# Optimization experiments

Hardware: AMD Instinct MI355X
Metric: run time of the kernel (lower is better)

Reference implementation:

```python
import jax, jax.numpy as jnp
import numpy as np

B, NQ, NK = 4, 2048, 2048
DQ = DK = DV = 512
H = 8
DS = DV // H  # 64


def _layernorm(x, g, b, eps=1e-5):
    m = jnp.mean(x, axis=-1, keepdims=True)
    v = jnp.var(x, axis=-1, keepdims=True)
    return (x - m) * jax.lax.rsqrt(v + eps) * g + b


def setup_inputs() -> dict:
    key = jax.random.key(0)
    ks = jax.random.split(key, 16)
    def lin(k, fan_in, fan_out):
        # torch nn.Linear default init: U(-1/sqrt(fan_in), 1/sqrt(fan_in))
        bound = 1.0 / np.sqrt(fan_in)
        k1, k2 = jax.random.split(k)
        W = jax.random.uniform(k1, (fan_in, fan_out), jnp.float32, -bound, bound)
        b = jax.random.uniform(k2, (fan_out,), jnp.float32, -bound, bound)
        return W, b
    Wq, bq = lin(ks[0], DQ, DV)
    Wk, bk = lin(ks[1], DK, DV)
    Wv, bv = lin(ks[2], DK, DV)
    W0, b0 = lin(ks[3], DV, DV)
    W1, b1 = lin(ks[4], DV, DV)
    # xavier_uniform for kp/vp of shape (1, DS): bound = sqrt(6/(1+DS))
    xb = np.sqrt(6.0 / (1 + DS))
    kp = jax.random.uniform(ks[5], (DS,), jnp.float32, -xb, xb)
    vp = jax.random.uniform(ks[6], (DS,), jnp.float32, -xb, xb)
    return {
        "Q": jax.random.normal(ks[7], (B, NQ, DQ), jnp.float32),
        "K": jax.random.normal(ks[8], (B, NK, DK), jnp.float32),
        "Kpos": jax.random.uniform(ks[9], (B, NQ, NK), jnp.float32),
        "Wq": Wq, "bq": bq, "Wk": Wk, "bk": bk, "Wv": Wv, "bv": bv,
        "kp": kp, "vp": vp,
        "W0": W0, "b0": b0, "W1": W1, "b1": b1,
        "g0": jnp.ones((DV,), jnp.float32), "be0": jnp.zeros((DV,), jnp.float32),
        "g1": jnp.ones((DV,), jnp.float32), "be1": jnp.zeros((DV,), jnp.float32),
    }


def reference(Q, K, Kpos, Wq, bq, Wk, bk, Wv, bv, kp, vp, W0, b0, W1, b1, g0, be0, g1, be1):
    Qp = Q @ Wq + bq                       # [B,NQ,DV]
    Kp = K @ Wk + bk                       # [B,NK,DV]
    Vp = K @ Wv + bv                       # [B,NK,DV]
    # head split (torch split/cat along batch == reshape to [B,N,H,DS])
    Qh = Qp.reshape(B, NQ, H, DS)
    Kh = Kp.reshape(B, NK, H, DS)
    Vh = Vp.reshape(B, NK, H, DS)
    scale = 1.0 / np.sqrt(DV)              # NOTE: original scales by sqrt(dim_V), not per-head dim
    scores = jnp.einsum('bqhd,bkhd->bhqk', Qh, Kh) * scale
    # ShawRE key bias: KE[b,h,q,k] = Kpos[b,q,k] * <Qh[b,q,h,:], kp>
    qkp = jnp.einsum('bqhd,d->bhq', Qh, kp)          # [B,H,NQ]
    scores = scores + Kpos[:, None, :, :] * qkp[:, :, :, None]
    A = jax.nn.softmax(scores, axis=-1)              # [B,H,NQ,NK]
    out = jnp.einsum('bhqk,bkhd->bqhd', A, Vh)       # [B,NQ,H,DS]
    # ShawRE value bias: VE[b,q,h,:] = (sum_k A*Kpos) * vp
    akp = jnp.einsum('bhqk,bqk->bhq', A, Kpos)       # [B,H,NQ]
    out = out + akp.transpose(0, 2, 1)[..., None] * vp
    O = (Qh + out).reshape(B, NQ, DV)
    O = _layernorm(O, g0, be0)
    resO = O
    O = jax.nn.relu(O @ W0 + b0)           # fc_o[0] with relu (numlayers=2)
    O = resO + jax.nn.relu(O @ W1 + b1)    # fc_o[-1] + residual
    O = _layernorm(O, g1, be1)
    return O
```

## Files before the change

kernel.cpp:

```cpp
#include <hip/hip_runtime.h>
#include <math.h>

#define Bx  4
#define NQx 2048
#define NKx 2048
#define Dx  512
#define Hx  8

typedef __attribute__((ext_vector_type(8))) __bf16 bf16x8;
typedef __attribute__((ext_vector_type(4))) float f32x4;
typedef __attribute__((ext_vector_type(16))) float f32x16;

typedef const __attribute__((address_space(1))) unsigned int* gas_ptr;
typedef __attribute__((address_space(3))) unsigned int* lds_ptr;

__device__ __forceinline__ void gload16(const void* g, void* l){
  __builtin_amdgcn_global_load_lds((gas_ptr)g, (lds_ptr)l, 16, 0, 0);
}

__device__ __forceinline__ unsigned short f2bf(float f){
  union { float f; unsigned int u; } v; v.f = f;
  unsigned int r = (v.u + 0x7FFFu + ((v.u >> 16) & 1u)) >> 16;
  return (unsigned short)r;
}
__device__ __forceinline__ float bf2f(unsigned short u){
  union { unsigned int u; float f; } v; v.u = ((unsigned int)u) << 16; return v.f;
}
__device__ __forceinline__ unsigned int cvtpk_bf16(float a, float b){
  unsigned int d;
  asm("v_cvt_pk_bf16_f32 %0, %1, %2" : "=v"(d) : "v"(a), "v"(b));
  return d;
}
__device__ __forceinline__ void plane32_swap(unsigned int& a, unsigned int& b){
  asm("v_permlane32_swap_b32 %0, %1" : "+v"(a), "+v"(b));
}
__device__ __forceinline__ float fexp2(float x){
  float d; asm("v_exp_f32 %0, %1" : "=v"(d) : "v"(x)); return d;
}
__device__ __forceinline__ float fmax3(float a, float b, float c){
  float d; asm("v_max3_f32 %0, %1, %2, %3" : "=v"(d) : "v"(a), "v"(b), "v"(c)); return d;
}

__global__ __launch_bounds__(256) void mab_wt(
    const float* __restrict__ Wq, const float* __restrict__ Wk, const float* __restrict__ Wv,
    const float* __restrict__ W0, const float* __restrict__ W1,
    unsigned short* __restrict__ Wt)
{
  __shared__ unsigned short T[64][72];
  const int z = blockIdx.z;
  const float* W = (z==0)?Wq:(z==1)?Wk:(z==2)?Wv:(z==3)?W0:W1;
  unsigned short* O = Wt + (size_t)z*512*512;
  const int k0 = blockIdx.x*64, n0 = blockIdx.y*64;
  const int tid = threadIdx.x;
  #pragma unroll
  for (int i=0;i<4;++i){
    int id = tid + i*256;
    int r = id>>4, c4 = id&15;
    float4 v = *(const float4*)(W + (size_t)(k0+r)*512 + n0 + c4*4);
    ushort4 o; o.x=f2bf(v.x); o.y=f2bf(v.y); o.z=f2bf(v.z); o.w=f2bf(v.w);
    *(ushort4*)&T[r][c4*4] = o;
  }
  __syncthreads();
  #pragma unroll
  for (int i=0;i<2;++i){
    int id = tid + i*256;
    int c = id>>3, r8 = id&7;
    union { unsigned short u[8]; uint4 v; } o;
    #pragma unroll
    for (int j=0;j<8;++j) o.u[j] = T[r8*8+j][c];
    *(uint4*)(O + (size_t)(n0+c)*512 + k0 + r8*8) = o.v;
  }
}

__global__ __launch_bounds__(256) void mab_vt(
    const unsigned short* __restrict__ Vp, unsigned short* __restrict__ Vpt)
{
  __shared__ unsigned short T[64][72];
  const int r0 = blockIdx.x*64;
  const int c0 = blockIdx.y*64;
  const int b  = blockIdx.z;
  const int tid = threadIdx.x;
  #pragma unroll
  for (int i=0;i<2;++i){
    int id = tid + i*256;
    int r = id>>3, c8 = id&7;
    *(uint4*)&T[r][c8*8] = *(const uint4*)(Vp + (size_t)(b*NKx + r0+r)*512 + c0 + c8*8);
  }
  __syncthreads();
  #pragma unroll
  for (int i=0;i<2;++i){
    int id = tid + i*256;
    int c = id>>3, r8 = id&7;
    union { unsigned short u[8]; uint4 v; } o;
    #pragma unroll
    for (int j=0;j<8;++j) o.u[j] = T[r8*8+j][c];
    *(uint4*)(Vpt + ((size_t)(b*512) + c0 + c)*NKx + r0 + r8*8) = o.v;
  }
}

__global__ __launch_bounds__(256) void mab_gemm_proj(
    const float* __restrict__ Qf, const float* __restrict__ Kf,
    const unsigned short* __restrict__ Wt,
    const float* __restrict__ bq, const float* __restrict__ bk, const float* __restrict__ bv,
    unsigned short* __restrict__ Cb, float kscale)
{
  __shared__ unsigned short As[128][64];
  __shared__ unsigned short Bs[128][64];
  const int z = blockIdx.z;
  const float* A = (z==0) ? Qf : Kf;
  const unsigned short* W = Wt + (size_t)z*512*512;
  const float* bias = (z==0)?bq:((z==1)?bk:bv);
  const float sc = (z==1) ? kscale : 1.0f;
  const int m0 = blockIdx.y*128, n0 = blockIdx.x*128;
  const int tid = threadIdx.x, w = tid>>6, lane = tid&63, g = lane>>4, q16 = lane&15;
  const int wr = w>>1, wc = w&1;

  f32x4 acc[4][4];
  #pragma unroll
  for (int m=0;m<4;++m)
    #pragma unroll
    for (int n=0;n<4;++n) acc[m][n] = (f32x4){0.f,0.f,0.f,0.f};

  float4 areg[8];
  #pragma unroll
  for (int i=0;i<8;++i){
    int id = i*256 + tid, row = id>>4, qc = id&15;
    areg[i] = *(const float4*)(A + (size_t)(m0+row)*512 + qc*4);
  }

  for (int k0 = 0; k0 < 512; k0 += 64){
    __syncthreads();
    #pragma unroll
    for (int i=0;i<8;++i){
      int id = i*256 + tid, row = id>>4, qc = id&15;
      unsigned int lo = cvtpk_bf16(areg[i].x, areg[i].y);
      unsigned int hi = cvtpk_bf16(areg[i].z, areg[i].w);
      unsigned int* dst = (unsigned int*)((char*)&As[0][0] + row*128
                          + ((qc>>1) ^ (row&7))*16 + (qc&1)*8);
      dst[0] = lo; dst[1] = hi;
    }
    #pragma unroll
    for (int i=0;i<4;++i){
      int o   = (w*4 + i)*1024 + lane*16;
      int row = o >> 7;
      int c   = (o >> 4) & 7;
      int cs  = c ^ (row & 7);
      gload16(W + (size_t)(n0+row)*512 + k0 + cs*8, (char*)&Bs[0][0] + (w*4+i)*1024);
    }
    __syncthreads();
    if (k0 + 64 < 512){
      #pragma unroll
      for (int i=0;i<8;++i){
        int id = i*256 + tid, row = id>>4, qc = id&15;
        areg[i] = *(const float4*)(A + (size_t)(m0+row)*512 + (k0+64) + qc*4);
      }
    }
    #pragma unroll
    for (int ks=0;ks<2;++ks){
      bf16x8 af[4], bfr[4];
      #pragma unroll
      for (int m=0;m<4;++m){
        int row = wr*64 + m*16 + q16;
        int c   = (ks*4 + g) ^ (row & 7);
        af[m] = *(const bf16x8*)((const char*)&As[0][0] + row*128 + c*16);
      }
      #pragma unroll
      for (int n=0;n<4;++n){
        int row = wc*64 + n*16 + q16;
        int c   = (ks*4 + g) ^ (row & 7);
        bfr[n] = *(const bf16x8*)((const char*)&Bs[0][0] + row*128 + c*16);
      }
      #pragma unroll
      for (int m=0;m<4;++m)
        #pragma unroll
        for (int n=0;n<4;++n)
          acc[m][n] = __builtin_amdgcn_mfma_f32_16x16x32_bf16(af[m], bfr[n], acc[m][n], 0,0,0);
    }
  }

  const size_t ZS = (size_t)8192*512;
  #pragma unroll
  for (int m=0;m<4;++m){
    const int rowl = wr*64 + m*16 + g*4;
    #pragma unroll
    for (int n=0;n<4;++n){
      const int col = n0 + wc*64 + n*16 + q16;
      const float bv2 = bias[col];
      #pragma unroll
      for (int r=0;r<4;++r){
        float v = (acc[m][n][r] + bv2) * sc;
        Cb[(size_t)z*ZS + (size_t)(m0 + rowl + r)*512 + col] = f2bf(v);
      }
    }
  }
}

__global__ __launch_bounds__(256) void mab_gemm_mfma(
    const unsigned short* __restrict__ A, const unsigned short* __restrict__ W,
    const float* __restrict__ bias, const float* __restrict__ res,
    unsigned short* __restrict__ Cb, float* __restrict__ Cf, int relu)
{
  __shared__ unsigned short As[128][64];
  __shared__ unsigned short Bs[128][64];
  const int m0 = blockIdx.y*128, n0 = blockIdx.x*128;
  const int tid = threadIdx.x, w = tid>>6, lane = tid&63, g = lane>>4, q16 = lane&15;
  const int wr = w>>1, wc = w&1;

  f32x4 acc[4][4];
  #pragma unroll
  for (int m=0;m<4;++m)
    #pragma unroll
    for (int n=0;n<4;++n) acc[m][n] = (f32x4){0.f,0.f,0.f,0.f};

  for (int k0 = 0; k0 < 512; k0 += 64){
    __syncthreads();
    #pragma unroll
    for (int i=0;i<4;++i){
      int o   = (w*4 + i)*1024 + lane*16;
      int row = o >> 7;
      int c   = (o >> 4) & 7;
      int cs  = c ^ (row & 7);
      gload16(A + (size_t)(m0+row)*512 + k0 + cs*8, (char*)&As[0][0] + (w*4+i)*1024);
      gload16(W + (size_t)(n0+row)*512 + k0 + cs*8, (char*)&Bs[0][0] + (w*4+i)*1024);
    }
    __syncthreads();
    #pragma unroll
    for (int ks=0;ks<2;++ks){
      bf16x8 af[4], bfr[4];
      #pragma unroll
      for (int m=0;m<4;++m){
        int row = wr*64 + m*16 + q16;
        int c   = (ks*4 + g) ^ (row & 7);
        af[m] = *(const bf16x8*)((const char*)&As[0][0] + row*128 + c*16);
      }
      #pragma unroll
      for (int n=0;n<4;++n){
        int row = wc*64 + n*16 + q16;
        int c   = (ks*4 + g) ^ (row & 7);
        bfr[n] = *(const bf16x8*)((const char*)&Bs[0][0] + row*128 + c*16);
      }
      #pragma unroll
      for (int m=0;m<4;++m)
        #pragma unroll
        for (int n=0;n<4;++n)
          acc[m][n] = __builtin_amdgcn_mfma_f32_16x16x32_bf16(af[m], bfr[n], acc[m][n], 0,0,0);
    }
  }

  #pragma unroll
  for (int m=0;m<4;++m){
    const int rowl = wr*64 + m*16 + g*4;
    #pragma unroll
    for (int n=0;n<4;++n){
      const int col = n0 + wc*64 + n*16 + q16;
      const float bv = bias[col];
      #pragma unroll
      for (int r=0;r<4;++r){
        float v = acc[m][n][r] + bv;
        if (relu) v = fmaxf(v, 0.f);
        size_t off = (size_t)(m0 + rowl + r)*512 + col;
        if (res) v += res[off];
        if (Cb) Cb[off] = f2bf(v);
        if (Cf) Cf[off] = v;
      }
    }
  }
}

__global__ __launch_bounds__(256) void mab_attn2(
    const unsigned short* __restrict__ Qp, const unsigned short* __restrict__ Kp,
    const unsigned short* __restrict__ Vpt,
    const float* __restrict__ Kpos, const float* __restrict__ kp, const float* __restrict__ vp,
    float* __restrict__ X)
{
  __shared__ unsigned short Kb[2][64][64];
  __shared__ unsigned short Vb[2][64][64];
  __shared__ unsigned short Qs[128][72];

  const int q0 = blockIdx.x*128;
  const int h  = blockIdx.y;
  const int b  = blockIdx.z;
  const int tid = threadIdx.x, w = tid>>6, lane = tid&63;
  const int q32 = lane & 31, hi = lane >> 5;

  const unsigned short* Qg = Qp + ((size_t)(b*NQx + q0))*Dx + h*64;
  const unsigned short* Kg = Kp + ((size_t)b*NKx)*Dx + h*64;
  const unsigned short* Vg = Vpt + ((size_t)(b*512) + h*64)*NKx;
  const float* KProw = Kpos + (size_t)b*NQx*NKx + (size_t)(q0 + w*32 + q32)*NKx;

  const int sr = lane>>3;
  const int sc = lane&7;

  #pragma unroll
  for (int i=0;i<2;++i){
    int r  = i*8 + sr;
    int cs = sc ^ (r & 7);
    gload16(Kg + (size_t)(w*16 + r)*Dx + cs*8, (char*)&Kb[0][0][0] + w*2048 + i*1024);
    gload16(Vg + (size_t)(w*16 + r)*NKx + cs*8, (char*)&Vb[0][0][0] + w*2048 + i*1024);
  }
  f32x4 kq[2][4];
  #pragma unroll
  for (int n=0;n<2;++n)
    #pragma unroll
    for (int a=0;a<4;++a)
      kq[n][a] = *(const f32x4*)(KProw + n*32 + a*8 + hi*4);
  #pragma unroll
  for (int i=0;i<4;++i){
    int id = tid + i*256;
    int r = id>>3, c8 = id&7;
    *(uint4*)&Qs[r][c8*8] = *(const uint4*)(Qg + (size_t)r*Dx + c8*8);
  }
  __syncthreads();

  bf16x8 qf[4];
  #pragma unroll
  for (int ds=0; ds<4; ++ds)
    qf[ds] = *(const bf16x8*)&Qs[w*32 + q32][ds*16 + hi*8];

  float qkp = 0.f;
  #pragma unroll
  for (int ds=0; ds<4; ++ds){
    union { bf16x8 v; unsigned short u[8]; } qa; qa.v = qf[ds];
    #pragma unroll
    for (int j=0;j<8;++j)
      qkp = fmaf(bf2f(qa.u[j]), kp[ds*16 + hi*8 + j], qkp);
  }
  qkp += __shfl_xor(qkp, 32);
  qkp *= 1.4426950408889634f;

  float m_i = -1e30f, l_i = 0.f, a_i = 0.f;
  f32x16 accT[2];
  #pragma unroll
  for (int db=0; db<2; ++db)
    #pragma unroll
    for (int r=0;r<16;++r) accT[db][r] = 0.f;

  const int NT = NKx/64;

  for (int kt = 0; kt < NT; ++kt){
    const int cur = kt & 1;
    const int k0 = kt*64;

    if (kt+1 < NT){
      const int k1 = k0 + 64;
      #pragma unroll
      for (int i=0;i<2;++i){
        int r  = i*8 + sr;
        int cs = sc ^ (r & 7);
        gload16(Kg + (size_t)(k1 + w*16 + r)*Dx + cs*8,
                (char*)&Kb[cur^1][0][0] + w*2048 + i*1024);
        gload16(Vg + (size_t)(w*16 + r)*NKx + k1 + cs*8,
                (char*)&Vb[cur^1][0][0] + w*2048 + i*1024);
      }
    }
    __builtin_amdgcn_sched_barrier(0);

    f32x16 sT[2];
    __builtin_amdgcn_s_setprio(1);
    #pragma unroll
    for (int n=0;n<2;++n){
      f32x16 c;
      #pragma unroll
      for (int r=0;r<16;++r) c[r] = 0.f;
      #pragma unroll
      for (int ds=0; ds<4; ++ds){
        int row = n*32 + q32;
        int cc  = (ds*2 + hi) ^ (q32 & 7);
        bf16x8 kf = *(const bf16x8*)((const char*)&Kb[cur][0][0] + row*128 + cc*16);
        c = __builtin_amdgcn_mfma_f32_32x32x16_bf16(kf, qf[ds], c, 0,0,0);
      }
      sT[n] = c;
    }
    __builtin_amdgcn_s_setprio(0);

    #pragma unroll
    for (int n=0;n<2;++n)
      #pragma unroll
      for (int r=0;r<16;++r)
        sT[n][r] = fmaf(kq[n][r>>2][r&3], qkp, sT[n][r]);

    float m0a = fmax3(sT[0][0], sT[0][1], sT[0][2]);
    float m0b = fmax3(sT[0][3], sT[0][4], sT[0][5]);
    float m0c = fmax3(sT[0][6], sT[0][7], sT[0][8]);
    float m0d = fmax3(sT[0][9], sT[0][10], sT[0][11]);
    float m0e = fmax3(sT[0][12], sT[0][13], sT[0][14]);
    float m1a = fmax3(sT[1][0], sT[1][1], sT[1][2]);
    float m1b = fmax3(sT[1][3], sT[1][4], sT[1][5]);
    float m1c = fmax3(sT[1][6], sT[1][7], sT[1][8]);
    float m1d = fmax3(sT[1][9], sT[1][10], sT[1][11]);
    float m1e = fmax3(sT[1][12], sT[1][13], sT[1][14]);
    float rm = fmax3(fmax3(m0a, m0b, m0c), fmax3(m0d, m0e, sT[0][15]),
                     fmax3(fmax3(m1a, m1b, m1c), fmax3(m1d, m1e, sT[1][15]), m_i));
    rm = fmaxf(rm, __shfl_xor(rm, 32));

    if (!__all(rm <= m_i + 11.544f)){
      float al = fexp2(m_i - rm);
      m_i = rm;
      l_i *= al; a_i *= al;
      #pragma unroll
      for (int db=0; db<2; ++db)
        #pragma unroll
        for (int r=0;r<16;++r) accT[db][r] *= al;
    }

    float ps = 0.f, pk = 0.f;
    #pragma unroll
    for (int n=0;n<2;++n)
      #pragma unroll
      for (int r=0;r<16;++r){
        float p = fexp2(sT[n][r] - m_i);
        sT[n][r] = p;
        ps += p;
        pk = fmaf(p, kq[n][r>>2][r&3], pk);
      }

    {
      const int kn = (kt+1 < NT) ? (k0 + 64) : k0;
      #pragma unroll
      for (int n=0;n<2;++n)
        #pragma unroll
        for (int a=0;a<4;++a)
          kq[n][a] = *(const f32x4*)(KProw + kn + n*32 + a*8 + hi*4);
    }

    ps += __shfl_xor(ps, 32);
    pk += __shfl_xor(pk, 32);
    l_i += ps; a_i += pk;

    union PW { unsigned int u[4]; bf16x8 v; } pa[4];
    #pragma unroll
    for (int n=0;n<2;++n){
      unsigned int w0 = cvtpk_bf16(sT[n][0],  sT[n][1]);
      unsigned int w1 = cvtpk_bf16(sT[n][2],  sT[n][3]);
      unsigned int w2 = cvtpk_bf16(sT[n][4],  sT[n][5]);
      unsigned int w3 = cvtpk_bf16(sT[n][6],  sT[n][7]);
      unsigned int w4 = cvtpk_bf16(sT[n][8],  sT[n][9]);
      unsigned int w5 = cvtpk_bf16(sT[n][10], sT[n][11]);
      unsigned int w6 = cvtpk_bf16(sT[n][12], sT[n][13]);
      unsigned int w7 = cvtpk_bf16(sT[n][14], sT[n][15]);
      plane32_swap(w0, w2);
      plane32_swap(w1, w3);
      plane32_swap(w4, w6);
      plane32_swap(w5, w7);
      pa[n*2+0].u[0]=w0; pa[n*2+0].u[1]=w1; pa[n*2+0].u[2]=w2; pa[n*2+0].u[3]=w3;
      pa[n*2+1].u[0]=w4; pa[n*2+1].u[1]=w5; pa[n*2+1].u[2]=w6; pa[n*2+1].u[3]=w7;
    }

    __builtin_amdgcn_s_setprio(1);
    #pragma unroll
    for (int st=0; st<4; ++st){
      #pragma unroll
      for (int db=0; db<2; ++db){
        int row = db*32 + q32;
        int cc  = (st*2 + hi) ^ (q32 & 7);
        bf16x8 vf = *(const bf16x8*)((const char*)&Vb[cur][0][0] + row*128 + cc*16);
        accT[db] = __builtin_amdgcn_mfma_f32_32x32x16_bf16(vf, pa[st].v, accT[db], 0,0,0);
      }
    }
    __builtin_amdgcn_s_setprio(0);

    asm volatile("s_waitcnt vmcnt(8)" ::: "memory");
    __builtin_amdgcn_s_barrier();
  }

  float inv = 1.0f / l_i;
  float aw  = a_i * inv;
  float* Xrow = X + ((size_t)(b*NQx + q0 + w*32 + q32))*Dx + h*64;
  #pragma unroll
  for (int db=0; db<2; ++db){
    #pragma unroll
    for (int a=0; a<4; ++a){
      int d0 = db*32 + a*8 + hi*4;
      f32x4 vpv = *(const f32x4*)(vp + d0);
      float4 o;
      o.x = fmaf(accT[db][a*4+0], inv, bf2f(Qs[w*32+q32][d0+0]) + aw*vpv[0]);
      o.y = fmaf(accT[db][a*4+1], inv, bf2f(Qs[w*32+q32][d0+1]) + aw*vpv[1]);
      o.z = fmaf(accT[db][a*4+2], inv, bf2f(Qs[w*32+q32][d0+2]) + aw*vpv[2]);
      o.w = fmaf(accT[db][a*4+3], inv, bf2f(Qs[w*32+q32][d0+3]) + aw*vpv[3]);
      *(float4*)(Xrow + d0) = o;
    }
  }
}

__global__ __launch_bounds__(256) void mab_ln2(
    const float* __restrict__ Xin, const float* __restrict__ g,
    const float* __restrict__ be, float* __restrict__ Yf, unsigned short* __restrict__ Yb)
{
  const int row = blockIdx.x;
  const int tid = threadIdx.x;
  const float* x = Xin + (size_t)row*Dx;
  float2 v = *(const float2*)(x + tid*2);
  float s  = v.x + v.y;
  float sq = fmaf(v.x,v.x, v.y*v.y);
  #pragma unroll
  for (int m=1; m<64; m<<=1){ s += __shfl_xor(s,m); sq += __shfl_xor(sq,m); }
  __shared__ float red[2][4];
  const int wid = tid>>6, lane = tid&63;
  if (lane==0){ red[0][wid]=s; red[1][wid]=sq; }
  __syncthreads();
  s  = red[0][0]+red[0][1]+red[0][2]+red[0][3];
  sq = red[1][0]+red[1][1]+red[1][2]+red[1][3];
  float mean = s*(1.0f/Dx);
  float var  = sq*(1.0f/Dx) - mean*mean;
  float rstd = rsqrtf(var + 1e-5f);
  float2 gg = *(const float2*)(g  + tid*2);
  float2 bb = *(const float2*)(be + tid*2);
  float2 o;
  o.x = (v.x-mean)*rstd*gg.x + bb.x;
  o.y = (v.y-mean)*rstd*gg.y + bb.y;
  if (Yf) *(float2*)(Yf + (size_t)row*Dx + tid*2) = o;
  if (Yb){
    ushort2 ob; ob.x = f2bf(o.x); ob.y = f2bf(o.y);
    *(ushort2*)(Yb + (size_t)row*Dx + tid*2) = ob;
  }
}

extern "C" void kernel_launch(void* const* d_in, const int* in_sizes, int n_in,
                              void* d_out, int out_size, void* d_ws, size_t ws_size,
                              hipStream_t stream)
{
  const float* Q    = (const float*)d_in[0];
  const float* K    = (const float*)d_in[1];
  const float* Kpos = (const float*)d_in[2];
  const float* Wq   = (const float*)d_in[3];
  const float* bq   = (const float*)d_in[4];
  const float* Wk   = (const float*)d_in[5];
  const float* bk   = (const float*)d_in[6];
  const float* Wv   = (const float*)d_in[7];
  const float* bv   = (const float*)d_in[8];
  const float* kp   = (const float*)d_in[9];
  const float* vp   = (const float*)d_in[10];
  const float* W0   = (const float*)d_in[11];
  const float* b0   = (const float*)d_in[12];
  const float* W1   = (const float*)d_in[13];
  const float* b1   = (const float*)d_in[14];
  const float* g0   = (const float*)d_in[15];
  const float* be0  = (const float*)d_in[16];
  const float* g1   = (const float*)d_in[17];
  const float* be1  = (const float*)d_in[18];
  float* out = (float*)d_out;
  char* wsb  = (char*)d_ws;

  const size_t MB = 1024*1024;
  unsigned short* Qp  = (unsigned short*)(wsb);
  unsigned short* Kp  = (unsigned short*)(wsb + 8*MB);
  unsigned short* Vp  = (unsigned short*)(wsb + 16*MB);
  float*          O0  = (float*)         (wsb + 24*MB);
  unsigned short* Vpt = (unsigned short*)(wsb + 40*MB);
  unsigned short* O0b = (unsigned short*)(wsb + 48*MB);
  unsigned short* Wt  = (unsigned short*)(wsb + 56*MB);
  unsigned short* T1  = Vp;

  const float kscale = 0.044194173824159216f * 1.4426950408889634f;

  mab_wt<<<dim3(8,8,5), 256, 0, stream>>>(Wq, Wk, Wv, W0, W1, Wt);
  mab_gemm_proj<<<dim3(4,64,3), 256, 0, stream>>>(Q, K, Wt, bq, bk, bv, Qp, kscale);
  mab_vt<<<dim3(32,8,4), 256, 0, stream>>>(Vp, Vpt);
  mab_attn2<<<dim3(16,8,4), 256, 0, stream>>>(Qp, Kp, Vpt, Kpos, kp, vp, out);
  mab_ln2<<<8192, 256, 0, stream>>>(out, g0, be0, O0, O0b);
  mab_gemm_mfma<<<dim3(4,64,1), 256, 0, stream>>>(
      O0b, Wt + (size_t)3*512*512, b0, nullptr, T1, nullptr, 1);
  mab_gemm_mfma<<<dim3(4,64,1), 256, 0, stream>>>(
      T1, Wt + (size_t)4*512*512, b1, O0, nullptr, out, 1);
  mab_ln2<<<8192, 256, 0, stream>>>(out, g1, be1, out, nullptr);
}
```

Measured before the change: 210.0 us.

## Split attention key range across wave pairs and merge partial softmax states

```diff
diff --git a/kernel.cpp b/kernel.cpp
--- a/kernel.cpp
+++ b/kernel.cpp
@@ -267,55 +267,50 @@
   }
 }
 
-__global__ __launch_bounds__(256) void mab_attn2(
+__global__ __launch_bounds__(256, 4) void mab_attn3(
     const unsigned short* __restrict__ Qp, const unsigned short* __restrict__ Kp,
     const unsigned short* __restrict__ Vpt,
     const float* __restrict__ Kpos, const float* __restrict__ kp, const float* __restrict__ vp,
     float* __restrict__ X)
 {
-  __shared__ unsigned short Kb[2][64][64];
-  __shared__ unsigned short Vb[2][64][64];
-  __shared__ unsigned short Qs[128][72];
-
-  const int q0 = blockIdx.x*128;
+  __shared__ __align__(16) char pool[32768];
+
+  const int q0 = blockIdx.x*64;
   const int h  = blockIdx.y;
   const int b  = blockIdx.z;
   const int tid = threadIdx.x, w = tid>>6, lane = tid&63;
   const int q32 = lane & 31, hi = lane >> 5;
+  const int g = w>>1;
+  const int qrow = (w&1)*32 + q32;
+
+  char* Kbase = pool + g*16384;
+  char* Vbase = pool + g*16384 + 8192;
 
   const unsigned short* Qg = Qp + ((size_t)(b*NQx + q0))*Dx + h*64;
   const unsigned short* Kg = Kp + ((size_t)b*NKx)*Dx + h*64;
   const unsigned short* Vg = Vpt + ((size_t)(b*512) + h*64)*NKx;
-  const float* KProw = Kpos + (size_t)b*NQx*NKx + (size_t)(q0 + w*32 + q32)*NKx;
-
-  const int sr = lane>>3;
-  const int sc = lane&7;
+  const float* KProw = Kpos + (size_t)b*NQx*NKx + (size_t)(q0 + qrow)*NKx;
+
+  const int krow0 = lane>>3, kch = lane&7;
+  const int vrow0 = lane>>2, vch = lane&3;
+  const int shalf = (w&1)*2;
 
   #pragma unroll
   for (int i=0;i<2;++i){
-    int r  = i*8 + sr;
-    int cs = sc ^ (r & 7);
-    gload16(Kg + (size_t)(w*16 + r)*Dx + cs*8, (char*)&Kb[0][0][0] + w*2048 + i*1024);
-    gload16(Vg + (size_t)(w*16 + r)*NKx + cs*8, (char*)&Vb[0][0][0] + w*2048 + i*1024);
-  }
-  f32x4 kq[2][4];
-  #pragma unroll
-  for (int n=0;n<2;++n)
-    #pragma unroll
-    for (int a=0;a<4;++a)
-      kq[n][a] = *(const f32x4*)(KProw + n*32 + a*8 + hi*4);
-  #pragma unroll
-  for (int i=0;i<4;++i){
-    int id = tid + i*256;
-    int r = id>>3, c8 = id&7;
-    *(uint4*)&Qs[r][c8*8] = *(const uint4*)(Qg + (size_t)r*Dx + c8*8);
-  }
-  __syncthreads();
-
+    int s = shalf + i;
+    int kr = s*8 + krow0;
+    int kcs = kch ^ (kr & 7);
+    gload16(Kg + (size_t)(g*32 + kr)*Dx + kcs*8, Kbase + s*1024);
+    int vr = s*16 + vrow0;
+    int vcs = vch ^ ((vr>>1) & 3);
+    gload16(Vg + (size_t)vr*NKx + g*32 + vcs*8, Vbase + s*1024);
+  }
+
+  const unsigned short* Qrowp = Qg + (size_t)qrow*Dx;
   bf16x8 qf[4];
   #pragma unroll
   for (int ds=0; ds<4; ++ds)
-    qf[ds] = *(const bf16x8*)&Qs[w*32 + q32][ds*16 + hi*8];
+    qf[ds] = *(const bf16x8*)(Qrowp + ds*16 + hi*8);
 
   float qkp = 0.f;
   #pragma unroll
@@ -335,62 +330,54 @@
     #pragma unroll
     for (int r=0;r<16;++r) accT[db][r] = 0.f;
 
-  const int NT = NKx/64;
-
-  for (int kt = 0; kt < NT; ++kt){
-    const int cur = kt & 1;
-    const int k0 = kt*64;
-
-    if (kt+1 < NT){
-      const int k1 = k0 + 64;
+  __syncthreads();
+
+  for (int t = 0; t < 32; ++t){
+    const int cur = t & 1;
+    const int k0g = t*64 + g*32;
+
+    f32x4 kq[4];
+    #pragma unroll
+    for (int a=0;a<4;++a)
+      kq[a] = *(const f32x4*)(KProw + k0g + a*8 + hi*4);
+
+    if (t < 31){
+      const int k1 = k0g + 64;
       #pragma unroll
       for (int i=0;i<2;++i){
-        int r  = i*8 + sr;
-        int cs = sc ^ (r & 7);
-        gload16(Kg + (size_t)(k1 + w*16 + r)*Dx + cs*8,
-                (char*)&Kb[cur^1][0][0] + w*2048 + i*1024);
-        gload16(Vg + (size_t)(w*16 + r)*NKx + k1 + cs*8,
-                (char*)&Vb[cur^1][0][0] + w*2048 + i*1024);
+        int s = shalf + i;
+        int kr = s*8 + krow0;
+        int kcs = kch ^ (kr & 7);
+        gload16(Kg + (size_t)(k1 + kr)*Dx + kcs*8, Kbase + (cur^1)*4096 + s*1024);
+        int vr = s*16 + vrow0;
+        int vcs = vch ^ ((vr>>1) & 3);
+        gload16(Vg + (size_t)vr*NKx + k1 + vcs*8, Vbase + (cur^1)*4096 + s*1024);
       }
     }
     __builtin_amdgcn_sched_barrier(0);
 
-    f32x16 sT[2];
+    f32x16 sT;
+    #pragma unroll
+    for (int r=0;r<16;++r) sT[r] = 0.f;
     __builtin_amdgcn_s_setprio(1);
     #pragma unroll
-    for (int n=0;n<2;++n){
-      f32x16 c;
-      #pragma unroll
-      for (int r=0;r<16;++r) c[r] = 0.f;
-      #pragma unroll
-      for (int ds=0; ds<4; ++ds){
-        int row = n*32 + q32;
-        int cc  = (ds*2 + hi) ^ (q32 & 7);
-        bf16x8 kf = *(const bf16x8*)((const char*)&Kb[cur][0][0] + row*128 + cc*16);
-        c = __builtin_amdgcn_mfma_f32_32x32x16_bf16(kf, qf[ds], c, 0,0,0);
-      }
-      sT[n] = c;
+    for (int ds=0; ds<4; ++ds){
+      int cc = (ds*2 + hi) ^ (q32 & 7);
+      bf16x8 kf = *(const bf16x8*)(Kbase + cur*4096 + q32*128 + cc*16);
+      sT = __builtin_amdgcn_mfma_f32_32x32x16_bf16(kf, qf[ds], sT, 0,0,0);
     }
     __builtin_amdgcn_s_setprio(0);
 
     #pragma unroll
-    for (int n=0;n<2;++n)
-      #pragma unroll
-      for (int r=0;r<16;++r)
-        sT[n][r] = fmaf(kq[n][r>>2][r&3], qkp, sT[n][r]);
-
-    float m0a = fmax3(sT[0][0], sT[0][1], sT[0][2]);
-    float m0b = fmax3(sT[0][3], sT[0][4], sT[0][5]);
-    float m0c = fmax3(sT[0][6], sT[0][7], sT[0][8]);
-    float m0d = fmax3(sT[0][9], sT[0][10], sT[0][11]);
-    float m0e = fmax3(sT[0][12], sT[0][13], sT[0][14]);
-    float m1a = fmax3(sT[1][0], sT[1][1], sT[1][2]);
-    float m1b = fmax3(sT[1][3], sT[1][4], sT[1][5]);
-    float m1c = fmax3(sT[1][6], sT[1][7], sT[1][8]);
-    float m1d = fmax3(sT[1][9], sT[1][10], sT[1][11]);
-    float m1e = fmax3(sT[1][12], sT[1][13], sT[1][14]);
-    float rm = fmax3(fmax3(m0a, m0b, m0c), fmax3(m0d, m0e, sT[0][15]),
-                     fmax3(fmax3(m1a, m1b, m1c), fmax3(m1d, m1e, sT[1][15]), m_i));
+    for (int r=0;r<16;++r)
+      sT[r] = fmaf(kq[r>>2][r&3], qkp, sT[r]);
+
+    float p0 = fmax3(sT[0],  sT[1],  sT[2]);
+    float p1 = fmax3(sT[3],  sT[4],  sT[5]);
+    float p2 = fmax3(sT[6],  sT[7],  sT[8]);
+    float p3 = fmax3(sT[9],  sT[10], sT[11]);
+    float p4 = fmax3(sT[12], sT[13], sT[14]);
+    float rm = fmax3(fmax3(p0, p1, p2), fmax3(p3, p4, sT[15]), m_i);
     rm = fmaxf(rm, __shfl_xor(rm, 32));
 
     if (!__all(rm <= m_i + 11.544f)){
@@ -405,78 +392,82 @@
 
     float ps = 0.f, pk = 0.f;
     #pragma unroll
-    for (int n=0;n<2;++n)
-      #pragma unroll
-      for (int r=0;r<16;++r){
-        float p = fexp2(sT[n][r] - m_i);
-        sT[n][r] = p;
-        ps += p;
-        pk = fmaf(p, kq[n][r>>2][r&3], pk);
-      }
-
-    {
-      const int kn = (kt+1 < NT) ? (k0 + 64) : k0;
-      #pragma unroll
-      for (int n=0;n<2;++n)
-        #pragma unroll
-        for (int a=0;a<4;++a)
-          kq[n][a] = *(const f32x4*)(KProw + kn + n*32 + a*8 + hi*4);
-    }
-
+    for (int r=0;r<16;++r){
+      float p = fexp2(sT[r] - m_i);
+      sT[r] = p;
+      ps += p;
+      pk = fmaf(p, kq[r>>2][r&3], pk);
+    }
     ps += __shfl_xor(ps, 32);
     pk += __shfl_xor(pk, 32);
     l_i += ps; a_i += pk;
 
-    union PW { unsigned int u[4]; bf16x8 v; } pa[4];
-    #pragma unroll
-    for (int n=0;n<2;++n){
-      unsigned int w0 = cvtpk_bf16(sT[n][0],  sT[n][1]);
-      unsigned int w1 = cvtpk_bf16(sT[n][2],  sT[n][3]);
-      unsigned int w2 = cvtpk_bf16(sT[n][4],  sT[n][5]);
-      unsigned int w3 = cvtpk_bf16(sT[n][6],  sT[n][7]);
-      unsigned int w4 = cvtpk_bf16(sT[n][8],  sT[n][9]);
-      unsigned int w5 = cvtpk_bf16(sT[n][10], sT[n][11]);
-      unsigned int w6 = cvtpk_bf16(sT[n][12], sT[n][13]);
-      unsigned int w7 = cvtpk_bf16(sT[n][14], sT[n][15]);
+    union PW { unsigned int u[4]; bf16x8 v; } pa[2];
+    {
+      unsigned int w0 = cvtpk_bf16(sT[0],  sT[1]);
+      unsigned int w1 = cvtpk_bf16(sT[2],  sT[3]);
+      unsigned int w2 = cvtpk_bf16(sT[4],  sT[5]);
+      unsigned int w3 = cvtpk_bf16(sT[6],  sT[7]);
+      unsigned int w4 = cvtpk_bf16(sT[8],  sT[9]);
+      unsigned int w5 = cvtpk_bf16(sT[10], sT[11]);
+      unsigned int w6 = cvtpk_bf16(sT[12], sT[13]);
+      unsigned int w7 = cvtpk_bf16(sT[14], sT[15]);
       plane32_swap(w0, w2);
       plane32_swap(w1, w3);
       plane32_swap(w4, w6);
       plane32_swap(w5, w7);
-      pa[n*2+0].u[0]=w0; pa[n*2+0].u[1]=w1; pa[n*2+0].u[2]=w2; pa[n*2+0].u[3]=w3;
-      pa[n*2+1].u[0]=w4; pa[n*2+1].u[1]=w5; pa[n*2+1].u[2]=w6; pa[n*2+1].u[3]=w7;
+      pa[0].u[0]=w0; pa[0].u[1]=w1; pa[0].u[2]=w2; pa[0].u[3]=w3;
+      pa[1].u[0]=w4; pa[1].u[1]=w5; pa[1].u[2]=w6; pa[1].u[3]=w7;
     }
 
     __builtin_amdgcn_s_setprio(1);
     #pragma unroll
-    for (int st=0; st<4; ++st){
+    for (int c2=0; c2<2; ++c2){
       #pragma unroll
       for (int db=0; db<2; ++db){
         int row = db*32 + q32;
-        int cc  = (st*2 + hi) ^ (q32 & 7);
-        bf16x8 vf = *(const bf16x8*)((const char*)&Vb[cur][0][0] + row*128 + cc*16);
-        accT[db] = __builtin_amdgcn_mfma_f32_32x32x16_bf16(vf, pa[st].v, accT[db], 0,0,0);
+        int cc  = (c2*2 + hi) ^ ((row>>1) & 3);
+        bf16x8 vf = *(const bf16x8*)(Vbase + cur*4096 + row*64 + cc*16);
+        accT[db] = __builtin_amdgcn_mfma_f32_32x32x16_bf16(vf, pa[c2].v, accT[db], 0,0,0);
       }
     }
     __builtin_amdgcn_s_setprio(0);
 
-    asm volatile("s_waitcnt vmcnt(8)" ::: "memory");
-    __builtin_amdgcn_s_barrier();
-  }
-
-  float inv = 1.0f / l_i;
-  float aw  = a_i * inv;
-  float* Xrow = X + ((size_t)(b*NQx + q0 + w*32 + q32))*Dx + h*64;
-  #pragma unroll
-  for (int db=0; db<2; ++db){
-    #pragma unroll
-    for (int a=0; a<4; ++a){
-      int d0 = db*32 + a*8 + hi*4;
+    __syncthreads();
+  }
+
+  __syncthreads();
+  float* mp = (float*)pool;
+  {
+    int slot = w*64 + lane;
+    float* ms = mp + slot*20;
+    int send = 1 - g;
+    #pragma unroll
+    for (int r=0;r<16;++r) ms[r] = accT[send][r];
+    ms[16] = m_i; ms[17] = l_i; ms[18] = a_i;
+  }
+  __syncthreads();
+  {
+    int pslot = (w^2)*64 + lane;
+    const float* pp = mp + pslot*20;
+    float pm = pp[16], pl = pp[17], pav = pp[18];
+    float mM = fmaxf(m_i, pm);
+    float alS = fexp2(m_i - mM), alP = fexp2(pm - mM);
+    float lM = fmaf(l_i, alS, pl*alP);
+    float aM = fmaf(a_i, alS, pav*alP);
+    float inv = 1.0f / lM;
+    float aw  = aM * inv;
+    float* Xrow = X + ((size_t)(b*NQx + q0 + qrow))*Dx + h*64;
+    #pragma unroll
+    for (int a2=0; a2<4; ++a2){
+      int d0 = g*32 + a2*8 + hi*4;
       f32x4 vpv = *(const f32x4*)(vp + d0);
+      ushort4 qh = *(const ushort4*)(Qrowp + d0);
       float4 o;
-      o.x = fmaf(accT[db][a*4+0], inv, bf2f(Qs[w*32+q32][d0+0]) + aw*vpv[0]);
-      o.y = fmaf(accT[db][a*4+1], inv, bf2f(Qs[w*32+q32][d0+1]) + aw*vpv[1]);
-      o.z = fmaf(accT[db][a*4+2], inv, bf2f(Qs[w*32+q32][d0+2]) + aw*vpv[2]);
-      o.w = fmaf(accT[db][a*4+3], inv, bf2f(Qs[w*32+q32][d0+3]) + aw*vpv[3]);
+      o.x = fmaf(fmaf(accT[g][a2*4+0], alS, pp[a2*4+0]*alP), inv, bf2f(qh.x) + aw*vpv[0]);
+      o.y = fmaf(fmaf(accT[g][a2*4+1], alS, pp[a2*4+1]*alP), inv, bf2f(qh.y) + aw*vpv[1]);
+      o.z = fmaf(fmaf(accT[g][a2*4+2], alS, pp[a2*4+2]*alP), inv, bf2f(qh.z) + aw*vpv[2]);
+      o.w = fmaf(fmaf(accT[g][a2*4+3], alS, pp[a2*4+3]*alP), inv, bf2f(qh.w) + aw*vpv[3]);
       *(float4*)(Xrow + d0) = o;
     }
   }
@@ -556,7 +547,7 @@
   mab_wt<<<dim3(8,8,5), 256, 0, stream>>>(Wq, Wk, Wv, W0, W1, Wt);
   mab_gemm_proj<<<dim3(4,64,3), 256, 0, stream>>>(Q, K, Wt, bq, bk, bv, Qp, kscale);
   mab_vt<<<dim3(32,8,4), 256, 0, stream>>>(Vp, Vpt);
-  mab_attn2<<<dim3(16,8,4), 256, 0, stream>>>(Qp, Kp, Vpt, Kpos, kp, vp, out);
+  mab_attn3<<<dim3(32,8,4), 256, 0, stream>>>(Qp, Kp, Vpt, Kpos, kp, vp, out);
   mab_ln2<<<8192, 256, 0, stream>>>(out, g0, be0, O0, O0b);
   mab_gemm_mfma<<<dim3(4,64,1), 256, 0, stream>>>(
       O0b, Wt + (size_t)3*512*512, b0, nullptr, T1, nullptr, 1);
```

Measured after the change: 217.8 us, median of 4. +3.7%, slower.

## Split attention KV loop across two wave groups and merge softmax partials

Applied to the files above, without the earlier changes.

```diff
diff --git a/kernel.cpp b/kernel.cpp
--- a/kernel.cpp
+++ b/kernel.cpp
@@ -267,55 +267,50 @@
   }
 }
 
-__global__ __launch_bounds__(256) void mab_attn2(
+__global__ __launch_bounds__(512, 4) void mab_attn4(
     const unsigned short* __restrict__ Qp, const unsigned short* __restrict__ Kp,
     const unsigned short* __restrict__ Vpt,
     const float* __restrict__ Kpos, const float* __restrict__ kp, const float* __restrict__ vp,
     float* __restrict__ X)
 {
-  __shared__ unsigned short Kb[2][64][64];
-  __shared__ unsigned short Vb[2][64][64];
-  __shared__ unsigned short Qs[128][72];
+  __shared__ __align__(16) char pool[65536];
 
   const int q0 = blockIdx.x*128;
   const int h  = blockIdx.y;
   const int b  = blockIdx.z;
   const int tid = threadIdx.x, w = tid>>6, lane = tid&63;
   const int q32 = lane & 31, hi = lane >> 5;
+  const int qg = w & 3;
+  const int kg = w >> 2;
+  const int qrow = qg*32 + q32;
+
+  char* Kbase = pool + kg*32768;
+  char* Vbase = pool + kg*32768 + 16384;
 
   const unsigned short* Qg = Qp + ((size_t)(b*NQx + q0))*Dx + h*64;
   const unsigned short* Kg = Kp + ((size_t)b*NKx)*Dx + h*64;
   const unsigned short* Vg = Vpt + ((size_t)(b*512) + h*64)*NKx;
-  const float* KProw = Kpos + (size_t)b*NQx*NKx + (size_t)(q0 + w*32 + q32)*NKx;
+  const float* KProw = Kpos + (size_t)b*NQx*NKx + (size_t)(q0 + qrow)*NKx;
 
   const int sr = lane>>3;
   const int sc = lane&7;
 
-  #pragma unroll
-  for (int i=0;i<2;++i){
-    int r  = i*8 + sr;
-    int cs = sc ^ (r & 7);
-    gload16(Kg + (size_t)(w*16 + r)*Dx + cs*8, (char*)&Kb[0][0][0] + w*2048 + i*1024);
-    gload16(Vg + (size_t)(w*16 + r)*NKx + cs*8, (char*)&Vb[0][0][0] + w*2048 + i*1024);
-  }
-  f32x4 kq[2][4];
-  #pragma unroll
-  for (int n=0;n<2;++n)
-    #pragma unroll
-    for (int a=0;a<4;++a)
-      kq[n][a] = *(const f32x4*)(KProw + n*32 + a*8 + hi*4);
-  #pragma unroll
-  for (int i=0;i<4;++i){
-    int id = tid + i*256;
-    int r = id>>3, c8 = id&7;
-    *(uint4*)&Qs[r][c8*8] = *(const uint4*)(Qg + (size_t)r*Dx + c8*8);
-  }
-  __syncthreads();
-
+  {
+    const int k0g = kg*64;
+    #pragma unroll
+    for (int i=0;i<2;++i){
+      int r  = qg*16 + i*8 + sr;
+      int cs = sc ^ (r & 7);
+      gload16(Kg + (size_t)(k0g + r)*Dx + cs*8, Kbase + qg*2048 + i*1024);
+      gload16(Vg + (size_t)r*NKx + k0g + cs*8, Vbase + qg*2048 + i*1024);
+    }
+  }
+
+  const unsigned short* Qrowp = Qg + (size_t)qrow*Dx;
   bf16x8 qf[4];
   #pragma unroll
   for (int ds=0; ds<4; ++ds)
-    qf[ds] = *(const bf16x8*)&Qs[w*32 + q32][ds*16 + hi*8];
+    qf[ds] = *(const bf16x8*)(Qrowp + ds*16 + hi*8);
 
   float qkp = 0.f;
   #pragma unroll
@@ -335,22 +330,29 @@
     #pragma unroll
     for (int r=0;r<16;++r) accT[db][r] = 0.f;
 
-  const int NT = NKx/64;
-
-  for (int kt = 0; kt < NT; ++kt){
-    const int cur = kt & 1;
-    const int k0 = kt*64;
-
-    if (kt+1 < NT){
-      const int k1 = k0 + 64;
+  __syncthreads();
+
+  for (int t = 0; t < 16; ++t){
+    const int cur = t & 1;
+    const int k0g = t*128 + kg*64;
+
+    f32x4 kq[2][4];
+    #pragma unroll
+    for (int n=0;n<2;++n)
+      #pragma unroll
+      for (int a=0;a<4;++a)
+        kq[n][a] = *(const f32x4*)(KProw + k0g + n*32 + a*8 + hi*4);
+
+    if (t < 15){
+      const int k1 = k0g + 128;
       #pragma unroll
       for (int i=0;i<2;++i){
-        int r  = i*8 + sr;
+        int r  = qg*16 + i*8 + sr;
         int cs = sc ^ (r & 7);
-        gload16(Kg + (size_t)(k1 + w*16 + r)*Dx + cs*8,
-                (char*)&Kb[cur^1][0][0] + w*2048 + i*1024);
-        gload16(Vg + (size_t)(w*16 + r)*NKx + k1 + cs*8,
-                (char*)&Vb[cur^1][0][0] + w*2048 + i*1024);
+        gload16(Kg + (size_t)(k1 + r)*Dx + cs*8,
+                Kbase + (cur^1)*8192 + qg*2048 + i*1024);
+        gload16(Vg + (size_t)r*NKx + k1 + cs*8,
+                Vbase + (cur^1)*8192 + qg*2048 + i*1024);
       }
     }
     __builtin_amdgcn_sched_barrier(0);
@@ -366,7 +368,7 @@
       for (int ds=0; ds<4; ++ds){
         int row = n*32 + q32;
         int cc  = (ds*2 + hi) ^ (q32 & 7);
-        bf16x8 kf = *(const bf16x8*)((const char*)&Kb[cur][0][0] + row*128 + cc*16);
+        bf16x8 kf = *(const bf16x8*)(Kbase + cur*8192 + row*128 + cc*16);
         c = __builtin_amdgcn_mfma_f32_32x32x16_bf16(kf, qf[ds], c, 0,0,0);
       }
       sT[n] = c;
@@ -413,16 +415,6 @@
         ps += p;
         pk = fmaf(p, kq[n][r>>2][r&3], pk);
       }
-
-    {
-      const int kn = (kt+1 < NT) ? (k0 + 64) : k0;
-      #pragma unroll
-      for (int n=0;n<2;++n)
-        #pragma unroll
-        for (int a=0;a<4;++a)
-          kq[n][a] = *(const f32x4*)(KProw + kn + n*32 + a*8 + hi*4);
-    }
-
     ps += __shfl_xor(ps, 32);
     pk += __shfl_xor(pk, 32);
     l_i += ps; a_i += pk;
@@ -453,30 +445,46 @@
       for (int db=0; db<2; ++db){
         int row = db*32 + q32;
         int cc  = (st*2 + hi) ^ (q32 & 7);
-        bf16x8 vf = *(const bf16x8*)((const char*)&Vb[cur][0][0] + row*128 + cc*16);
+        bf16x8 vf = *(const bf16x8*)(Vbase + cur*8192 + row*128 + cc*16);
         accT[db] = __builtin_amdgcn_mfma_f32_32x32x16_bf16(vf, pa[st].v, accT[db], 0,0,0);
       }
     }
     __builtin_amdgcn_s_setprio(0);
 
-    asm volatile("s_waitcnt vmcnt(8)" ::: "memory");
-    __builtin_amdgcn_s_barrier();
-  }
-
-  float inv = 1.0f / l_i;
-  float aw  = a_i * inv;
-  float* Xrow = X + ((size_t)(b*NQx + q0 + w*32 + q32))*Dx + h*64;
-  #pragma unroll
-  for (int db=0; db<2; ++db){
-    #pragma unroll
-    for (int a=0; a<4; ++a){
-      int d0 = db*32 + a*8 + hi*4;
+    __syncthreads();
+  }
+
+  float* mp = (float*)pool;
+  {
+    int slot = w*64 + lane;
+    float* ms = mp + slot*20;
+    int send = 1 - kg;
+    #pragma unroll
+    for (int r=0;r<16;++r) ms[r] = accT[send][r];
+    ms[16] = m_i; ms[17] = l_i; ms[18] = a_i;
+  }
+  __syncthreads();
+  {
+    int pslot = (w^4)*64 + lane;
+    const float* pp = mp + pslot*20;
+    float pm = pp[16], pl = pp[17], pav = pp[18];
+    float mM = fmaxf(m_i, pm);
+    float alS = fexp2(m_i - mM), alP = fexp2(pm - mM);
+    float lM = fmaf(l_i, alS, pl*alP);
+    float aM = fmaf(a_i, alS, pav*alP);
+    float inv = 1.0f / lM;
+    float aw  = aM * inv;
+    float* Xrow = X + ((size_t)(b*NQx + q0 + qrow))*Dx + h*64;
+    #pragma unroll
+    for (int a2=0; a2<4; ++a2){
+      int d0 = kg*32 + a2*8 + hi*4;
       f32x4 vpv = *(const f32x4*)(vp + d0);
+      ushort4 qh = *(const ushort4*)(Qrowp + d0);
       float4 o;
-      o.x = fmaf(accT[db][a*4+0], inv, bf2f(Qs[w*32+q32][d0+0]) + aw*vpv[0]);
-      o.y = fmaf(accT[db][a*4+1], inv, bf2f(Qs[w*32+q32][d0+1]) + aw*vpv[1]);
-      o.z = fmaf(accT[db][a*4+2], inv, bf2f(Qs[w*32+q32][d0+2]) + aw*vpv[2]);
-      o.w = fmaf(accT[db][a*4+3], inv, bf2f(Qs[w*32+q32][d0+3]) + aw*vpv[3]);
+      o.x = fmaf(fmaf(accT[kg][a2*4+0], alS, pp[a2*4+0]*alP), inv, bf2f(qh.x) + aw*vpv[0]);
+      o.y = fmaf(fmaf(accT[kg][a2*4+1], alS, pp[a2*4+1]*alP), inv, bf2f(qh.y) + aw*vpv[1]);
+      o.z = fmaf(fmaf(accT[kg][a2*4+2], alS, pp[a2*4+2]*alP), inv, bf2f(qh.z) + aw*vpv[2]);
+      o.w = fmaf(fmaf(accT[kg][a2*4+3], alS, pp[a2*4+3]*alP), inv, bf2f(qh.w) + aw*vpv[3]);
       *(float4*)(Xrow + d0) = o;
     }
   }
@@ -556,7 +564,7 @@
   mab_wt<<<dim3(8,8,5), 256, 0, stream>>>(Wq, Wk, Wv, W0, W1, Wt);
   mab_gemm_proj<<<dim3(4,64,3), 256, 0, stream>>>(Q, K, Wt, bq, bk, bv, Qp, kscale);
   mab_vt<<<dim3(32,8,4), 256, 0, stream>>>(Vp, Vpt);
-  mab_attn2<<<dim3(16,8,4), 256, 0, stream>>>(Qp, Kp, Vpt, Kpos, kp, vp, out);
+  mab_attn4<<<dim3(16,8,4), 512, 0, stream>>>(Qp, Kp, Vpt, Kpos, kp, vp, out);
   mab_ln2<<<8192, 256, 0, stream>>>(out, g0, be0, O0, O0b);
   mab_gemm_mfma<<<dim3(4,64,1), 256, 0, stream>>>(
       O0b, Wt + (size_t)3*512*512, b0, nullptr, T1, nullptr, 1);
```

After: 279.9 us. 33.3% more time.

## Restructure attention so one block covers all heads and shares Kpos through LDS

Applied to the files above, without the earlier changes.

```diff
diff --git a/kernel.cpp b/kernel.cpp
--- a/kernel.cpp
+++ b/kernel.cpp
@@ -267,55 +267,34 @@
   }
 }
 
-__global__ __launch_bounds__(256) void mab_attn2(
+__global__ __launch_bounds__(512, 2) void mab_attn5(
     const unsigned short* __restrict__ Qp, const unsigned short* __restrict__ Kp,
     const unsigned short* __restrict__ Vpt,
     const float* __restrict__ Kpos, const float* __restrict__ kp, const float* __restrict__ vp,
     float* __restrict__ X)
 {
-  __shared__ unsigned short Kb[2][64][64];
-  __shared__ unsigned short Vb[2][64][64];
-  __shared__ unsigned short Qs[128][72];
-
-  const int q0 = blockIdx.x*128;
-  const int h  = blockIdx.y;
-  const int b  = blockIdx.z;
+  __shared__ __align__(16) float KQ[2][2048];
+
+  const int b  = blockIdx.x;
+  const int q0 = blockIdx.y*32;
   const int tid = threadIdx.x, w = tid>>6, lane = tid&63;
   const int q32 = lane & 31, hi = lane >> 5;
+  const int h = w;
 
   const unsigned short* Qg = Qp + ((size_t)(b*NQx + q0))*Dx + h*64;
   const unsigned short* Kg = Kp + ((size_t)b*NKx)*Dx + h*64;
   const unsigned short* Vg = Vpt + ((size_t)(b*512) + h*64)*NKx;
-  const float* KProw = Kpos + (size_t)b*NQx*NKx + (size_t)(q0 + w*32 + q32)*NKx;
-
-  const int sr = lane>>3;
-  const int sc = lane&7;
-
-  #pragma unroll
-  for (int i=0;i<2;++i){
-    int r  = i*8 + sr;
-    int cs = sc ^ (r & 7);
-    gload16(Kg + (size_t)(w*16 + r)*Dx + cs*8, (char*)&Kb[0][0][0] + w*2048 + i*1024);
-    gload16(Vg + (size_t)(w*16 + r)*NKx + cs*8, (char*)&Vb[0][0][0] + w*2048 + i*1024);
-  }
-  f32x4 kq[2][4];
-  #pragma unroll
-  for (int n=0;n<2;++n)
-    #pragma unroll
-    for (int a=0;a<4;++a)
-      kq[n][a] = *(const f32x4*)(KProw + n*32 + a*8 + hi*4);
-  #pragma unroll
-  for (int i=0;i<4;++i){
-    int id = tid + i*256;
-    int r = id>>3, c8 = id&7;
-    *(uint4*)&Qs[r][c8*8] = *(const uint4*)(Qg + (size_t)r*Dx + c8*8);
-  }
-  __syncthreads();
-
+  const float* KPg = Kpos + (size_t)b*NQx*NKx + (size_t)q0*NKx;
+
+  const int prow = tid>>4;
+  const int pc4  = tid&15;
+  const int pchunk = pc4 ^ (prow & 7);
+
+  const unsigned short* Qrowp = Qg + (size_t)q32*Dx;
   bf16x8 qf[4];
   #pragma unroll
   for (int ds=0; ds<4; ++ds)
-    qf[ds] = *(const bf16x8*)&Qs[w*32 + q32][ds*16 + hi*8];
+    qf[ds] = *(const bf16x8*)(Qrowp + ds*16 + hi*8);
 
   float qkp = 0.f;
   #pragma unroll
@@ -335,24 +314,36 @@
     #pragma unroll
     for (int r=0;r<16;++r) accT[db][r] = 0.f;
 
+  {
+    float4 kv0 = *(const float4*)(KPg + (size_t)prow*NKx + pc4*4);
+    *(float4*)((char*)&KQ[0][0] + prow*256 + pchunk*16) = kv0;
+  }
+  bf16x8 kfA[2][4], kfB[2][4];
+  #pragma unroll
+  for (int n=0;n<2;++n)
+    #pragma unroll
+    for (int ds=0; ds<4; ++ds)
+      kfA[n][ds] = *(const bf16x8*)(Kg + (size_t)(n*32 + q32)*Dx + ds*16 + hi*8);
+  __syncthreads();
+
   const int NT = NKx/64;
 
-  for (int kt = 0; kt < NT; ++kt){
-    const int cur = kt & 1;
-    const int k0 = kt*64;
-
-    if (kt+1 < NT){
-      const int k1 = k0 + 64;
-      #pragma unroll
-      for (int i=0;i<2;++i){
-        int r  = i*8 + sr;
-        int cs = sc ^ (r & 7);
-        gload16(Kg + (size_t)(k1 + w*16 + r)*Dx + cs*8,
-                (char*)&Kb[cur^1][0][0] + w*2048 + i*1024);
-        gload16(Vg + (size_t)(w*16 + r)*NKx + k1 + cs*8,
-                (char*)&Vb[cur^1][0][0] + w*2048 + i*1024);
-      }
-    }
+  auto body = [&](int t, bf16x8 (&kfC)[2][4], bf16x8 (&kfN)[2][4]){
+    const int k0 = t*64;
+    const int kn = (t+1 < NT) ? (k0 + 64) : k0;
+
+    #pragma unroll
+    for (int n=0;n<2;++n)
+      #pragma unroll
+      for (int ds=0; ds<4; ++ds)
+        kfN[n][ds] = *(const bf16x8*)(Kg + (size_t)(kn + n*32 + q32)*Dx + ds*16 + hi*8);
+    bf16x8 vf[4][2];
+    #pragma unroll
+    for (int st=0; st<4; ++st)
+      #pragma unroll
+      for (int db=0; db<2; ++db)
+        vf[st][db] = *(const bf16x8*)(Vg + (size_t)(db*32 + q32)*NKx + k0 + st*16 + hi*8);
+    float4 knv = *(const float4*)(KPg + (size_t)prow*NKx + kn + pc4*4);
     __builtin_amdgcn_sched_barrier(0);
 
     f32x16 sT[2];
@@ -363,15 +354,20 @@
       #pragma unroll
       for (int r=0;r<16;++r) c[r] = 0.f;
       #pragma unroll
-      for (int ds=0; ds<4; ++ds){
-        int row = n*32 + q32;
-        int cc  = (ds*2 + hi) ^ (q32 & 7);
-        bf16x8 kf = *(const bf16x8*)((const char*)&Kb[cur][0][0] + row*128 + cc*16);
-        c = __builtin_amdgcn_mfma_f32_32x32x16_bf16(kf, qf[ds], c, 0,0,0);
-      }
+      for (int ds=0; ds<4; ++ds)
+        c = __builtin_amdgcn_mfma_f32_32x32x16_bf16(kfC[n][ds], qf[ds], c, 0,0,0);
       sT[n] = c;
     }
     __builtin_amdgcn_s_setprio(0);
+
+    f32x4 kq[2][4];
+    #pragma unroll
+    for (int n=0;n<2;++n)
+      #pragma unroll
+      for (int a=0;a<4;++a){
+        int chunk = (n*8 + a*2 + hi) ^ (q32 & 7);
+        kq[n][a] = *(const f32x4*)((const char*)&KQ[t&1][0] + q32*256 + chunk*16);
+      }
 
     #pragma unroll
     for (int n=0;n<2;++n)
@@ -413,16 +409,6 @@
         ps += p;
         pk = fmaf(p, kq[n][r>>2][r&3], pk);
       }
-
-    {
-      const int kn = (kt+1 < NT) ? (k0 + 64) : k0;
-      #pragma unroll
-      for (int n=0;n<2;++n)
-        #pragma unroll
-        for (int a=0;a<4;++a)
-          kq[n][a] = *(const f32x4*)(KProw + kn + n*32 + a*8 + hi*4);
-    }
-
     ps += __shfl_xor(ps, 32);
     pk += __shfl_xor(pk, 32);
     l_i += ps; a_i += pk;
@@ -450,33 +436,35 @@
     #pragma unroll
     for (int st=0; st<4; ++st){
       #pragma unroll
-      for (int db=0; db<2; ++db){
-        int row = db*32 + q32;
-        int cc  = (st*2 + hi) ^ (q32 & 7);
-        bf16x8 vf = *(const bf16x8*)((const char*)&Vb[cur][0][0] + row*128 + cc*16);
-        accT[db] = __builtin_amdgcn_mfma_f32_32x32x16_bf16(vf, pa[st].v, accT[db], 0,0,0);
-      }
+      for (int db=0; db<2; ++db)
+        accT[db] = __builtin_amdgcn_mfma_f32_32x32x16_bf16(vf[st][db], pa[st].v, accT[db], 0,0,0);
     }
     __builtin_amdgcn_s_setprio(0);
 
-    asm volatile("s_waitcnt vmcnt(8)" ::: "memory");
-    __builtin_amdgcn_s_barrier();
+    *(float4*)((char*)&KQ[(t+1)&1][0] + prow*256 + pchunk*16) = knv;
+    __syncthreads();
+  };
+
+  for (int t = 0; t < NT; t += 2){
+    body(t,   kfA, kfB);
+    body(t+1, kfB, kfA);
   }
 
   float inv = 1.0f / l_i;
   float aw  = a_i * inv;
-  float* Xrow = X + ((size_t)(b*NQx + q0 + w*32 + q32))*Dx + h*64;
+  float* Xrow = X + ((size_t)(b*NQx + q0 + q32))*Dx + h*64;
   #pragma unroll
   for (int db=0; db<2; ++db){
     #pragma unroll
-    for (int a=0; a<4; ++a){
-      int d0 = db*32 + a*8 + hi*4;
+    for (int a2=0; a2<4; ++a2){
+      int d0 = db*32 + a2*8 + hi*4;
       f32x4 vpv = *(const f32x4*)(vp + d0);
+      ushort4 qh = *(const ushort4*)(Qrowp + d0);
       float4 o;
-      o.x = fmaf(accT[db][a*4+0], inv, bf2f(Qs[w*32+q32][d0+0]) + aw*vpv[0]);
-      o.y = fmaf(accT[db][a*4+1], inv, bf2f(Qs[w*32+q32][d0+1]) + aw*vpv[1]);
-      o.z = fmaf(accT[db][a*4+2], inv, bf2f(Qs[w*32+q32][d0+2]) + aw*vpv[2]);
-      o.w = fmaf(accT[db][a*4+3], inv, bf2f(Qs[w*32+q32][d0+3]) + aw*vpv[3]);
+      o.x = fmaf(accT[db][a2*4+0], inv, bf2f(qh.x) + aw*vpv[0]);
+      o.y = fmaf(accT[db][a2*4+1], inv, bf2f(qh.y) + aw*vpv[1]);
+      o.z = fmaf(accT[db][a2*4+2], inv, bf2f(qh.z) + aw*vpv[2]);
+      o.w = fmaf(accT[db][a2*4+3], inv, bf2f(qh.w) + aw*vpv[3]);
       *(float4*)(Xrow + d0) = o;
     }
   }
@@ -556,7 +544,7 @@
   mab_wt<<<dim3(8,8,5), 256, 0, stream>>>(Wq, Wk, Wv, W0, W1, Wt);
   mab_gemm_proj<<<dim3(4,64,3), 256, 0, stream>>>(Q, K, Wt, bq, bk, bv, Qp, kscale);
   mab_vt<<<dim3(32,8,4), 256, 0, stream>>>(Vp, Vpt);
-  mab_attn2<<<dim3(16,8,4), 256, 0, stream>>>(Qp, Kp, Vpt, Kpos, kp, vp, out);
+  mab_attn5<<<dim3(4,64), 512, 0, stream>>>(Qp, Kp, Vpt, Kpos, kp, vp, out);
   mab_ln2<<<8192, 256, 0, stream>>>(out, g0, be0, O0, O0b);
   mab_gemm_mfma<<<dim3(4,64,1), 256, 0, stream>>>(
       O0b, Wt + (size_t)3*512*512, b0, nullptr, T1, nullptr, 1);
```

Result: slower. 257.2 us (+22.5%).
